# Kernel optimization log

Hardware: AMD Instinct MI355X
Metric: run time of the kernel (lower is better)

## Reference

```python
import jax, jax.numpy as jnp
import numpy as np

# --- static config (matches init_kwargs) ---
B, N, M = 128, 32, 32
C_IMG, NUM_HIDDEN, NUM_CLASSES = 1, 16, 3
INPUT_DIM = C_IMG + NUM_HIDDEN + NUM_CLASSES          # 20
OUT_DIM = NUM_HIDDEN + NUM_CLASSES + 2                # 21 (moving -> 2 action channels)
C_STATE = INPUT_DIM - C_IMG                           # 19
N_NEO, M_NEO = N - 2, M - 2                           # size_neo=None -> N-2
N_ACTIVE, M_ACTIVE = N - 2, M - 2
ITERATIONS = 10
IN_FEAT = 9 * INPUT_DIM + 2                           # 182, position='current'
THRESH = 0.0007


def setup_inputs() -> dict:
    key = jax.random.key(0)
    ks = jax.random.split(key, 7)
    images = jax.random.uniform(ks[0], (B, N, M, C_IMG), dtype=jnp.float32)
    W1 = jax.random.normal(ks[1], (IN_FEAT, 30), dtype=jnp.float32) * 0.08
    b1 = jnp.zeros((30,), jnp.float32)
    W2 = jax.random.normal(ks[2], (30, 30), dtype=jnp.float32) * 0.18
    b2 = jnp.zeros((30,), jnp.float32)
    W3 = jax.random.normal(ks[3], (30, OUT_DIM), dtype=jnp.float32) * 0.18
    b3 = jnp.zeros((OUT_DIM,), jnp.float32)
    return {"images": images, "W1": W1, "b1": b1, "W2": W2, "b2": b2, "W3": W3, "b3": b3}


def _custom_round(a):
    # positive -> +1, negative -> -1 (with deadzone |a| <= 0.0007 -> 0)
    return jnp.where(a > THRESH, 1, jnp.where(a < -THRESH, -1, 0)).astype(jnp.int32)


def _run(images, W1, b1, W2, b2, W3, b3):
    dx = jnp.arange(3)
    b_idx = jnp.arange(B)[:, None, None, None, None]        # (B,1,1,1,1)
    # fixed 3x3 windows into state (comms): state[x:x+3, y:y+3]
    sr = (jnp.arange(N_NEO)[:, None] + dx)[:, None, :, None]  # (Nn,1,3,1)
    sc = (jnp.arange(M_NEO)[:, None] + dx)[None, :, None, :]  # (1,Mn,1,3)
    half_n = N // 2
    half_m = M // 2

    # initial perception matrix: identity grid (N_neo == N_active)
    gx, gy = jnp.meshgrid(jnp.arange(N_NEO), jnp.arange(M_NEO), indexing="ij")
    perc0 = jnp.broadcast_to(jnp.stack([gx, gy], -1).astype(jnp.int32), (B, N_NEO, M_NEO, 2))
    state0 = jnp.zeros((B, N, M, C_STATE), jnp.float32)
    guesses0 = jnp.zeros((B * N_NEO * M_NEO, OUT_DIM), jnp.float32)

    def step(carry, _):
        state, perc, _ = carry
        px = perc[..., 0]  # (B,Nn,Mn) int32
        py = perc[..., 1]
        # dynamic 3x3 image patches at (px, py)
        rows = px[..., None, None] + dx[:, None]            # (B,Nn,Mn,3,1)
        cols = py[..., None, None] + dx[None, :]            # (B,Nn,Mn,1,3)
        perc_patch = images[b_idx, rows, cols, :]           # (B,Nn,Mn,3,3,C_IMG)
        comms = state[:, sr, sc, :]                          # (B,Nn,Mn,3,3,C_STATE)
        feat = jnp.concatenate([perc_patch, comms], axis=-1)  # (B,Nn,Mn,3,3,INPUT_DIM)
        feat = feat.reshape(B * N_NEO * M_NEO, 9 * INPUT_DIM)
        # position='current' features
        pos_x = ((px - half_n) / half_n).astype(jnp.float32).reshape(-1, 1)
        pos_y = ((py - half_m) / half_m).astype(jnp.float32).reshape(-1, 1)
        inp = jnp.concatenate([feat, pos_x, pos_y], axis=-1)  # (B*Nn*Mn, 182)
        h = jax.nn.relu(inp @ W1 + b1)
        h = jax.nn.relu(h @ W2 + b2)
        guesses = h @ W3 + b3                                 # (B*Nn*Mn, 21)
        outputs = guesses.reshape(B, N_NEO, M_NEO, OUT_DIM)
        state = state.at[:, 1:1 + N_NEO, 1:1 + M_NEO, :].add(outputs[..., :C_STATE])
        # movement: round actions to {-1,0,1}, add, clip to [0, N_active-1]
        delta = _custom_round(outputs[..., -2:])
        perc = jnp.clip(perc + delta, 0, N_ACTIVE - 1)
        return (state, perc, guesses), None

    (state, perc, guesses), _ = jax.lax.scan(step, (state0, perc0, guesses0), None, length=ITERATIONS)
    class_state = state[:, 1:1 + N_NEO, 1:1 + M_NEO, -NUM_CLASSES:]
    return class_state, guesses


def reference(images, W1, b1, W2, b2, W3, b3):
    return _run(images, W1, b1, W2, b2, W3, b3)
```

## Files before the change

kernel.cpp:

```cpp
#include <hip/hip_runtime.h>

#define B_      128
#define NPIX    32
#define NNEO    30
#define CSTATE  19
#define OUTD    21
#define ITERS   10
#define THRESHV 0.0007f

#define STATE_ELEMS (B_ * NPIX * NPIX * CSTATE)
#define NCELLS      (B_ * NNEO * NNEO)
#define CLASS_ELEMS (NCELLS * 3)

__global__ void nca_init(float* __restrict__ stateA, float* __restrict__ stateB,
                         int* __restrict__ perc) {
    int idx = blockIdx.x * blockDim.x + threadIdx.x;
    int stride = gridDim.x * blockDim.x;
    for (int i = idx; i < STATE_ELEMS; i += stride) {
        stateA[i] = 0.0f;
        stateB[i] = 0.0f;
    }
    for (int i = idx; i < NCELLS; i += stride) {
        int cell = i % (NNEO * NNEO);
        perc[2 * i + 0] = cell / NNEO;
        perc[2 * i + 1] = cell % NNEO;
    }
}

__global__ __launch_bounds__(256, 2)
void nca_step(const float* __restrict__ img,
              const float* __restrict__ W1, const float* __restrict__ b1,
              const float* __restrict__ W2, const float* __restrict__ b2,
              const float* __restrict__ W3, const float* __restrict__ b3,
              const float* __restrict__ state_old, float* __restrict__ state_new,
              int* perc, float* __restrict__ guesses_out, int write_guesses) {
    __shared__ float s_state[10 * NPIX * CSTATE];
    __shared__ float s_img[NPIX * NPIX];

    const int b   = blockIdx.y;
    const int rg  = blockIdx.x;
    const int i0  = rg * 8;
    const int nr  = (rg == 3) ? 6 : 8;
    const int tid = threadIdx.x;

    const int srows  = (32 - i0 < 10) ? (32 - i0) : 10;
    const int nstate4 = srows * NPIX * CSTATE / 4;
    const float4* gstate4 =
        (const float4*)(state_old + ((size_t)b * NPIX + i0) * NPIX * CSTATE);
    float4* s_state4 = (float4*)s_state;
    for (int t = tid; t < nstate4; t += 256) s_state4[t] = gstate4[t];
    const float4* gimg4 = (const float4*)(img + (size_t)b * NPIX * NPIX);
    float4* s_img4 = (float4*)s_img;
    if (tid < NPIX * NPIX / 4) s_img4[tid] = gimg4[tid];
    __syncthreads();

    const int cells = nr * NNEO;
    if (tid >= cells) return;

    const int r = tid / NNEO;
    const int j = tid % NNEO;
    const int i = i0 + r;
    const int cell = (b * NNEO + i) * NNEO + j;

    int px = perc[2 * cell + 0];
    int py = perc[2 * cell + 1];

    float h1[30];
#pragma unroll
    for (int q = 0; q < 30; q++) h1[q] = b1[q];

    for (int pr = 0; pr < 3; pr++) {
        for (int pc = 0; pc < 3; pc++) {
            const int p9 = pr * 3 + pc;
            const float iv = s_img[(px + pr) * NPIX + (py + pc)];
            {
                const float* __restrict__ wr = W1 + (p9 * 20 + 0) * 30;
#pragma unroll
                for (int q = 0; q < 30; q++) h1[q] += iv * wr[q];
            }
            const int sbase = ((r + pr) * NPIX + (j + pc)) * CSTATE;
            for (int ch = 0; ch < CSTATE; ch++) {
                const float v = s_state[sbase + ch];
                const float* __restrict__ wr = W1 + (p9 * 20 + 1 + ch) * 30;
#pragma unroll
                for (int q = 0; q < 30; q++) h1[q] += v * wr[q];
            }
        }
    }
    {
        const float posx = (float)(px - 16) * (1.0f / 16.0f);
        const float posy = (float)(py - 16) * (1.0f / 16.0f);
        const float* __restrict__ wx = W1 + 180 * 30;
        const float* __restrict__ wy = W1 + 181 * 30;
#pragma unroll
        for (int q = 0; q < 30; q++) h1[q] += posx * wx[q];
#pragma unroll
        for (int q = 0; q < 30; q++) h1[q] += posy * wy[q];
    }
#pragma unroll
    for (int q = 0; q < 30; q++) h1[q] = fmaxf(h1[q], 0.0f);

    float h2[30];
#pragma unroll
    for (int q = 0; q < 30; q++) h2[q] = b2[q];
    for (int k = 0; k < 30; k++) {
        const float v = h1[k];
        const float* __restrict__ wr = W2 + k * 30;
#pragma unroll
        for (int q = 0; q < 30; q++) h2[q] += v * wr[q];
    }
#pragma unroll
    for (int q = 0; q < 30; q++) h2[q] = fmaxf(h2[q], 0.0f);

    float o[21];
#pragma unroll
    for (int c = 0; c < 21; c++) o[c] = b3[c];
    for (int k = 0; k < 30; k++) {
        const float v = h2[k];
        const float* __restrict__ wr = W3 + k * 21;
#pragma unroll
        for (int c = 0; c < 21; c++) o[c] += v * wr[c];
    }

    const int lcenter = ((r + 1) * NPIX + (j + 1)) * CSTATE;
    float* __restrict__ ns =
        state_new + (((size_t)b * NPIX + (i + 1)) * NPIX + (j + 1)) * CSTATE;
#pragma unroll
    for (int ch = 0; ch < CSTATE; ch++) ns[ch] = s_state[lcenter + ch] + o[ch];

    if (write_guesses) {
        float* __restrict__ g = guesses_out + (size_t)cell * OUTD;
#pragma unroll
        for (int c = 0; c < OUTD; c++) g[c] = o[c];
    }

    int dxm = (o[19] > THRESHV) ? 1 : ((o[19] < -THRESHV) ? -1 : 0);
    int dym = (o[20] > THRESHV) ? 1 : ((o[20] < -THRESHV) ? -1 : 0);
    px += dxm; py += dym;
    px = (px < 0) ? 0 : ((px > NNEO - 1) ? NNEO - 1 : px);
    py = (py < 0) ? 0 : ((py > NNEO - 1) ? NNEO - 1 : py);
    perc[2 * cell + 0] = px;
    perc[2 * cell + 1] = py;
}

__global__ void nca_extract(const float* __restrict__ state, float* __restrict__ out) {
    int idx = blockIdx.x * blockDim.x + threadIdx.x;
    if (idx >= CLASS_ELEMS) return;
    int cc = idx % 3;
    int rest = idx / 3;
    int j = rest % NNEO; rest /= NNEO;
    int i = rest % NNEO;
    int b = rest / NNEO;
    out[idx] = state[(((size_t)b * NPIX + (i + 1)) * NPIX + (j + 1)) * CSTATE + 16 + cc];
}

extern "C" void kernel_launch(void* const* d_in, const int* in_sizes, int n_in,
                              void* d_out, int out_size, void* d_ws, size_t ws_size,
                              hipStream_t stream) {
    const float* img = (const float*)d_in[0];
    const float* W1  = (const float*)d_in[1];
    const float* b1  = (const float*)d_in[2];
    const float* W2  = (const float*)d_in[3];
    const float* b2  = (const float*)d_in[4];
    const float* W3  = (const float*)d_in[5];
    const float* b3  = (const float*)d_in[6];

    float* out = (float*)d_out;
    float* class_out   = out;
    float* guesses_out = out + CLASS_ELEMS;

    float* stateA = (float*)d_ws;
    float* stateB = stateA + STATE_ELEMS;
    int*   perc   = (int*)(stateB + STATE_ELEMS);

    nca_init<<<1024, 256, 0, stream>>>(stateA, stateB, perc);

    for (int t = 0; t < ITERS; t++) {
        const float* so = (t & 1) ? stateB : stateA;
        float*       sn = (t & 1) ? stateA : stateB;
        nca_step<<<dim3(4, B_), 256, 0, stream>>>(
            img, W1, b1, W2, b2, W3, b3, so, sn, perc, guesses_out,
            (t == ITERS - 1) ? 1 : 0);
    }
    nca_extract<<<(CLASS_ELEMS + 255) / 256, 256, 0, stream>>>(stateA, class_out);
}
```

Before: 379.8 us.

## Split each cell's MLP across two threads and specialize first/last steps

Each cell's MLP now runs on two threads, each computing half of the hidden and output units, with activations exchanged through shared memory. Blocks grow to 512 threads, which doubles the parallelism over a grid of only 512 blocks. Templated first and last step kernels skip state loads and the state term at t=0 (the state is all zeros there), fuse the class extraction into the final step, and skip the state write on the last step. Init now zeroes only the border cells and no longer writes perc. The cost is extra syncs, shared-memory traffic, and some redundant work in the idle lanes of the last row group.

New measurement: 369.6 us. 2.7% less time.

```diff
diff --git a/kernel.cpp b/kernel.cpp
--- a/kernel.cpp
+++ b/kernel.cpp
@@ -12,146 +12,195 @@
 #define NCELLS      (B_ * NNEO * NNEO)
 #define CLASS_ELEMS (NCELLS * 3)
 
-__global__ void nca_init(float* __restrict__ stateA, float* __restrict__ stateB,
-                         int* __restrict__ perc) {
+__global__ void nca_init(float* __restrict__ stateA, float* __restrict__ stateB) {
     int idx = blockIdx.x * blockDim.x + threadIdx.x;
-    int stride = gridDim.x * blockDim.x;
-    for (int i = idx; i < STATE_ELEMS; i += stride) {
-        stateA[i] = 0.0f;
-        stateB[i] = 0.0f;
-    }
-    for (int i = idx; i < NCELLS; i += stride) {
-        int cell = i % (NNEO * NNEO);
-        perc[2 * i + 0] = cell / NNEO;
-        perc[2 * i + 1] = cell % NNEO;
-    }
+    const int total = B_ * 124 * CSTATE;
+    if (idx >= total) return;
+    int c  = idx % CSTATE;
+    int t2 = idx / CSTATE;
+    int cell = t2 % 124;
+    int b    = t2 / 124;
+    int i, j;
+    if (cell < 32)      { i = 0;  j = cell; }
+    else if (cell < 64) { i = 31; j = cell - 32; }
+    else { int k = cell - 64; i = 1 + (k >> 1); j = (k & 1) ? 31 : 0; }
+    size_t off = (((size_t)b * NPIX + i) * NPIX + j) * CSTATE + c;
+    stateA[off] = 0.0f;
+    stateB[off] = 0.0f;
 }
 
-__global__ __launch_bounds__(256, 2)
+template<bool FIRST, bool LAST>
+__global__ __launch_bounds__(512, 4)
 void nca_step(const float* __restrict__ img,
               const float* __restrict__ W1, const float* __restrict__ b1,
               const float* __restrict__ W2, const float* __restrict__ b2,
               const float* __restrict__ W3, const float* __restrict__ b3,
               const float* __restrict__ state_old, float* __restrict__ state_new,
-              int* perc, float* __restrict__ guesses_out, int write_guesses) {
+              int* perc, float* __restrict__ guesses_out,
+              float* __restrict__ class_out) {
     __shared__ float s_state[10 * NPIX * CSTATE];
     __shared__ float s_img[NPIX * NPIX];
+    __shared__ float s_h[240 * 30];
 
     const int b   = blockIdx.y;
     const int rg  = blockIdx.x;
     const int i0  = rg * 8;
     const int nr  = (rg == 3) ? 6 : 8;
     const int tid = threadIdx.x;
-
-    const int srows  = (32 - i0 < 10) ? (32 - i0) : 10;
-    const int nstate4 = srows * NPIX * CSTATE / 4;
-    const float4* gstate4 =
-        (const float4*)(state_old + ((size_t)b * NPIX + i0) * NPIX * CSTATE);
-    float4* s_state4 = (float4*)s_state;
-    for (int t = tid; t < nstate4; t += 256) s_state4[t] = gstate4[t];
-    const float4* gimg4 = (const float4*)(img + (size_t)b * NPIX * NPIX);
-    float4* s_img4 = (float4*)s_img;
-    if (tid < NPIX * NPIX / 4) s_img4[tid] = gimg4[tid];
+    const int half = __builtin_amdgcn_readfirstlane(tid >> 8);
+    const int cell = tid & 255;
+
+    if (!FIRST) {
+        const int srows = (32 - i0 < 10) ? (32 - i0) : 10;
+        const int n4 = srows * NPIX * CSTATE / 4;
+        const float4* gstate4 =
+            (const float4*)(state_old + ((size_t)b * NPIX + i0) * NPIX * CSTATE);
+        float4* s_state4 = (float4*)s_state;
+        for (int t = tid; t < n4; t += 512) s_state4[t] = gstate4[t];
+    }
+    if (tid < NPIX * NPIX / 4) {
+        ((float4*)s_img)[tid] = ((const float4*)(img + (size_t)b * NPIX * NPIX))[tid];
+    }
     __syncthreads();
 
     const int cells = nr * NNEO;
-    if (tid >= cells) return;
-
-    const int r = tid / NNEO;
-    const int j = tid % NNEO;
-    const int i = i0 + r;
-    const int cell = (b * NNEO + i) * NNEO + j;
-
-    int px = perc[2 * cell + 0];
-    int py = perc[2 * cell + 1];
-
-    float h1[30];
-#pragma unroll
-    for (int q = 0; q < 30; q++) h1[q] = b1[q];
-
-    for (int pr = 0; pr < 3; pr++) {
-        for (int pc = 0; pc < 3; pc++) {
-            const int p9 = pr * 3 + pc;
-            const float iv = s_img[(px + pr) * NPIX + (py + pc)];
-            {
-                const float* __restrict__ wr = W1 + (p9 * 20 + 0) * 30;
-#pragma unroll
-                for (int q = 0; q < 30; q++) h1[q] += iv * wr[q];
-            }
-            const int sbase = ((r + pr) * NPIX + (j + pc)) * CSTATE;
-            for (int ch = 0; ch < CSTATE; ch++) {
-                const float v = s_state[sbase + ch];
-                const float* __restrict__ wr = W1 + (p9 * 20 + 1 + ch) * 30;
-#pragma unroll
-                for (int q = 0; q < 30; q++) h1[q] += v * wr[q];
-            }
-        }
-    }
+    const bool active = cell < cells;
+
+    int r = 0, j = 0, i = 0, gcell = 0, px = 0, py = 0;
+    if (active) {
+        r = cell / NNEO;
+        j = cell % NNEO;
+        i = i0 + r;
+        gcell = (b * NNEO + i) * NNEO + j;
+        if (FIRST) { px = i; py = j; }
+        else       { px = perc[2 * gcell]; py = perc[2 * gcell + 1]; }
+    }
+
+    float h1[15];
     {
+        const float* __restrict__ bb = b1 + 15 * half;
+#pragma unroll
+        for (int q = 0; q < 15; q++) h1[q] = bb[q];
+    }
+    if (active) {
+        for (int pr = 0; pr < 3; pr++) {
+            for (int pc = 0; pc < 3; pc++) {
+                const int p9 = pr * 3 + pc;
+                const float iv = s_img[(px + pr) * NPIX + (py + pc)];
+                {
+                    const float* __restrict__ wr = W1 + (p9 * 20) * 30 + 15 * half;
+#pragma unroll
+                    for (int q = 0; q < 15; q++) h1[q] += iv * wr[q];
+                }
+                if (!FIRST) {
+                    const int sbase = ((r + pr) * NPIX + (j + pc)) * CSTATE;
+                    float fv[CSTATE];
+#pragma unroll
+                    for (int ch = 0; ch < CSTATE; ch++) fv[ch] = s_state[sbase + ch];
+                    for (int ch = 0; ch < CSTATE; ch++) {
+                        const float* __restrict__ wr =
+                            W1 + (p9 * 20 + 1 + ch) * 30 + 15 * half;
+#pragma unroll
+                        for (int q = 0; q < 15; q++) h1[q] += fv[ch] * wr[q];
+                    }
+                }
+            }
+        }
         const float posx = (float)(px - 16) * (1.0f / 16.0f);
         const float posy = (float)(py - 16) * (1.0f / 16.0f);
-        const float* __restrict__ wx = W1 + 180 * 30;
-        const float* __restrict__ wy = W1 + 181 * 30;
-#pragma unroll
-        for (int q = 0; q < 30; q++) h1[q] += posx * wx[q];
-#pragma unroll
-        for (int q = 0; q < 30; q++) h1[q] += posy * wy[q];
-    }
-#pragma unroll
-    for (int q = 0; q < 30; q++) h1[q] = fmaxf(h1[q], 0.0f);
-
-    float h2[30];
-#pragma unroll
-    for (int q = 0; q < 30; q++) h2[q] = b2[q];
-    for (int k = 0; k < 30; k++) {
-        const float v = h1[k];
-        const float* __restrict__ wr = W2 + k * 30;
-#pragma unroll
-        for (int q = 0; q < 30; q++) h2[q] += v * wr[q];
-    }
-#pragma unroll
-    for (int q = 0; q < 30; q++) h2[q] = fmaxf(h2[q], 0.0f);
-
-    float o[21];
-#pragma unroll
-    for (int c = 0; c < 21; c++) o[c] = b3[c];
-    for (int k = 0; k < 30; k++) {
-        const float v = h2[k];
-        const float* __restrict__ wr = W3 + k * 21;
-#pragma unroll
-        for (int c = 0; c < 21; c++) o[c] += v * wr[c];
-    }
-
-    const int lcenter = ((r + 1) * NPIX + (j + 1)) * CSTATE;
-    float* __restrict__ ns =
-        state_new + (((size_t)b * NPIX + (i + 1)) * NPIX + (j + 1)) * CSTATE;
-#pragma unroll
-    for (int ch = 0; ch < CSTATE; ch++) ns[ch] = s_state[lcenter + ch] + o[ch];
-
-    if (write_guesses) {
-        float* __restrict__ g = guesses_out + (size_t)cell * OUTD;
-#pragma unroll
-        for (int c = 0; c < OUTD; c++) g[c] = o[c];
-    }
-
-    int dxm = (o[19] > THRESHV) ? 1 : ((o[19] < -THRESHV) ? -1 : 0);
-    int dym = (o[20] > THRESHV) ? 1 : ((o[20] < -THRESHV) ? -1 : 0);
-    px += dxm; py += dym;
-    px = (px < 0) ? 0 : ((px > NNEO - 1) ? NNEO - 1 : px);
-    py = (py < 0) ? 0 : ((py > NNEO - 1) ? NNEO - 1 : py);
-    perc[2 * cell + 0] = px;
-    perc[2 * cell + 1] = py;
-}
-
-__global__ void nca_extract(const float* __restrict__ state, float* __restrict__ out) {
-    int idx = blockIdx.x * blockDim.x + threadIdx.x;
-    if (idx >= CLASS_ELEMS) return;
-    int cc = idx % 3;
-    int rest = idx / 3;
-    int j = rest % NNEO; rest /= NNEO;
-    int i = rest % NNEO;
-    int b = rest / NNEO;
-    out[idx] = state[(((size_t)b * NPIX + (i + 1)) * NPIX + (j + 1)) * CSTATE + 16 + cc];
+        const float* __restrict__ wx = W1 + 180 * 30 + 15 * half;
+        const float* __restrict__ wy = W1 + 181 * 30 + 15 * half;
+#pragma unroll
+        for (int q = 0; q < 15; q++) h1[q] += posx * wx[q];
+#pragma unroll
+        for (int q = 0; q < 15; q++) h1[q] += posy * wy[q];
+#pragma unroll
+        for (int q = 0; q < 15; q++) h1[q] = fmaxf(h1[q], 0.0f);
+#pragma unroll
+        for (int q = 0; q < 15; q++) s_h[cell * 30 + 15 * half + q] = h1[q];
+    }
+    __syncthreads();
+
+    float h2[15];
+    {
+        const float* __restrict__ bb = b2 + 15 * half;
+#pragma unroll
+        for (int q = 0; q < 15; q++) h2[q] = bb[q];
+    }
+    if (active) {
+        float a1[30];
+#pragma unroll
+        for (int k = 0; k < 30; k++) a1[k] = s_h[cell * 30 + k];
+        for (int k = 0; k < 30; k++) {
+            const float* __restrict__ wr = W2 + k * 30 + 15 * half;
+#pragma unroll
+            for (int q = 0; q < 15; q++) h2[q] += a1[k] * wr[q];
+        }
+#pragma unroll
+        for (int q = 0; q < 15; q++) h2[q] = fmaxf(h2[q], 0.0f);
+    }
+    __syncthreads();
+    if (active) {
+#pragma unroll
+        for (int q = 0; q < 15; q++) s_h[cell * 30 + 15 * half + q] = h2[q];
+    }
+    __syncthreads();
+
+    const int c0   = half ? 11 : 0;
+    const int nout = half ? 10 : 11;
+    float o[11];
+#pragma unroll
+    for (int c = 0; c < 11; c++) o[c] = (c < nout) ? b3[c0 + c] : 0.0f;
+    if (active) {
+        float a2[30];
+#pragma unroll
+        for (int k = 0; k < 30; k++) a2[k] = s_h[cell * 30 + k];
+        for (int k = 0; k < 30; k++) {
+            const float* __restrict__ wr = W3 + k * 21 + c0;
+            if (half) {
+#pragma unroll
+                for (int c = 0; c < 10; c++) o[c] += a2[k] * wr[c];
+            } else {
+#pragma unroll
+                for (int c = 0; c < 11; c++) o[c] += a2[k] * wr[c];
+            }
+        }
+
+        const int lcenter = ((r + 1) * NPIX + (j + 1)) * CSTATE;
+        if (!LAST) {
+            float* __restrict__ ns =
+                state_new + (((size_t)b * NPIX + (i + 1)) * NPIX + (j + 1)) * CSTATE;
+            if (half == 0) {
+#pragma unroll
+                for (int c = 0; c < 11; c++)
+                    ns[c] = (FIRST ? 0.0f : s_state[lcenter + c]) + o[c];
+            } else {
+#pragma unroll
+                for (int c = 0; c < 8; c++)
+                    ns[11 + c] = (FIRST ? 0.0f : s_state[lcenter + 11 + c]) + o[c];
+                int dxm = (o[8] > THRESHV) ? 1 : ((o[8] < -THRESHV) ? -1 : 0);
+                int dym = (o[9] > THRESHV) ? 1 : ((o[9] < -THRESHV) ? -1 : 0);
+                px += dxm; py += dym;
+                px = (px < 0) ? 0 : ((px > NNEO - 1) ? NNEO - 1 : px);
+                py = (py < 0) ? 0 : ((py > NNEO - 1) ? NNEO - 1 : py);
+                perc[2 * gcell + 0] = px;
+                perc[2 * gcell + 1] = py;
+            }
+        } else {
+            float* __restrict__ g = guesses_out + (size_t)gcell * OUTD;
+            if (half == 0) {
+#pragma unroll
+                for (int c = 0; c < 11; c++) g[c] = o[c];
+            } else {
+#pragma unroll
+                for (int c = 0; c < 10; c++) g[11 + c] = o[c];
+                float* __restrict__ cs = class_out + (size_t)gcell * 3;
+#pragma unroll
+                for (int cc = 0; cc < 3; cc++)
+                    cs[cc] = s_state[lcenter + 16 + cc] + o[5 + cc];
+            }
+        }
+    }
 }
 
 extern "C" void kernel_launch(void* const* d_in, const int* in_sizes, int n_in,
@@ -173,14 +222,24 @@
     float* stateB = stateA + STATE_ELEMS;
     int*   perc   = (int*)(stateB + STATE_ELEMS);
 
-    nca_init<<<1024, 256, 0, stream>>>(stateA, stateB, perc);
-
+    {
+        const int total = B_ * 124 * CSTATE;
+        nca_init<<<(total + 255) / 256, 256, 0, stream>>>(stateA, stateB);
+    }
+
+    const dim3 grid(4, B_);
     for (int t = 0; t < ITERS; t++) {
         const float* so = (t & 1) ? stateB : stateA;
         float*       sn = (t & 1) ? stateA : stateB;
-        nca_step<<<dim3(4, B_), 256, 0, stream>>>(
-            img, W1, b1, W2, b2, W3, b3, so, sn, perc, guesses_out,
-            (t == ITERS - 1) ? 1 : 0);
-    }
-    nca_extract<<<(CLASS_ELEMS + 255) / 256, 256, 0, stream>>>(stateA, class_out);
+        if (t == 0) {
+            nca_step<true, false><<<grid, 512, 0, stream>>>(
+                img, W1, b1, W2, b2, W3, b3, so, sn, perc, guesses_out, class_out);
+        } else if (t == ITERS - 1) {
+            nca_step<false, true><<<grid, 512, 0, stream>>>(
+                img, W1, b1, W2, b2, W3, b3, so, sn, perc, guesses_out, class_out);
+        } else {
+            nca_step<false, false><<<grid, 512, 0, stream>>>(
+                img, W1, b1, W2, b2, W3, b3, so, sn, perc, guesses_out, class_out);
+        }
+    }
 }
```
